# Performance work log

Hardware: AMD Instinct MI355X
Metric: run time of the kernel (lower is better)

Reference implementation:

```python
import jax, jax.numpy as jnp
import numpy as np

NUM_LAYERS = 3
HIDDEN = 64
NUM_CLASSES = 4096
LN_EPS = 1e-5


def setup_inputs() -> dict:
    key = jax.random.key(0)
    ks = jax.random.split(key, 8)
    B, N, E, H = 8, NUM_CLASSES, 131072, HIDDEN
    node_features = jax.random.normal(ks[0], (B, N, H), dtype=jnp.float32)
    edge_indices = jax.random.randint(ks[1], (B, 2, E), 0, N, dtype=jnp.int64)
    edge_attrs = jax.random.normal(ks[2], (B, E, H), dtype=jnp.float32)
    # GraphConvolutionLayer params (xavier_uniform weight, zero bias) per layer
    limit = np.sqrt(6.0 / (H + H)).astype(np.float32)
    W = jax.random.uniform(ks[3], (NUM_LAYERS, H, H), minval=-limit, maxval=limit, dtype=jnp.float32)
    b = jnp.zeros((NUM_LAYERS, H), dtype=jnp.float32)
    gamma = jnp.ones((NUM_LAYERS, H), dtype=jnp.float32)
    beta = jnp.zeros((NUM_LAYERS, H), dtype=jnp.float32)
    global_emb = 0.02 * jax.random.normal(ks[4], (N, H), dtype=jnp.float32)
    return {
        "node_features": node_features,
        "edge_indices": edge_indices,
        "edge_attrs": edge_attrs,
        "W": W,
        "b": b,
        "gamma": gamma,
        "beta": beta,
        "global_emb": global_emb,
    }


def _layer_norm(x, g, bt):
    mu = jnp.mean(x, axis=-1, keepdims=True)
    var = jnp.mean((x - mu) ** 2, axis=-1, keepdims=True)
    return (x - mu) * jax.lax.rsqrt(var + LN_EPS) * g + bt


def reference(node_features, edge_indices, edge_attrs, W, b, gamma, beta, global_emb):
    N = node_features.shape[1]

    def per_graph(x0, ei, ea):
        # presence mask computed on raw node features [N, 1]
        presence = (jnp.sum(x0, axis=1) != 0).astype(x0.dtype)[:, None]
        src, dst = ei[0], ei[1]
        x = x0
        for i in range(NUM_LAYERS):
            residual = x
            h = x @ W[i]                                   # [N, H]
            msg = h[src] * ea                              # gather + edge gate [E, H]
            out = jax.ops.segment_sum(msg, dst, num_segments=N) + b[i]
            out = jax.nn.relu(out)
            out = _layer_norm(out, gamma[i], beta[i])
            x = out + residual if i > 0 else out
        return x * presence + global_emb * (1.0 - presence)

    return jax.vmap(per_graph)(node_features, edge_indices, edge_attrs)
```

## Files before the change

### kernel.cpp

```cpp
#include <hip/hip_runtime.h>

#define GB 8
#define GN 4096
#define GH 64
#define GE 131072
#define LN_EPS 1e-5f
#define NBIN (GB * GN)
#define TOTE (GB * GE)

static __device__ __forceinline__ unsigned short f2bf(float f) {
    union { float f; unsigned int u; } v; v.f = f;
    unsigned int u = v.u;
    return (unsigned short)((u + 0x7FFFu + ((u >> 16) & 1u)) >> 16);
}
static __device__ __forceinline__ void bf2x(unsigned int u, float& lo, float& hi) {
    union { float f; unsigned int i; } a, b;
    a.i = u << 16; b.i = u & 0xFFFF0000u;
    lo = a.f; hi = b.f;
}
static __device__ __forceinline__ void fma8(uint4 ev, uint4 hv, float4& a0, float4& a1) {
    float el, eh, hl, hh;
    bf2x(ev.x, el, eh); bf2x(hv.x, hl, hh);
    a0.x = fmaf(el, hl, a0.x); a0.y = fmaf(eh, hh, a0.y);
    bf2x(ev.y, el, eh); bf2x(hv.y, hl, hh);
    a0.z = fmaf(el, hl, a0.z); a0.w = fmaf(eh, hh, a0.w);
    bf2x(ev.z, el, eh); bf2x(hv.z, hl, hh);
    a1.x = fmaf(el, hl, a1.x); a1.y = fmaf(eh, hh, a1.y);
    bf2x(ev.w, el, eh); bf2x(hv.w, hl, hh);
    a1.z = fmaf(el, hl, a1.z); a1.w = fmaf(eh, hh, a1.w);
}

__global__ void k_init(const float* __restrict__ nf, float* __restrict__ pres) {
    int w = (blockIdx.x * blockDim.x + threadIdx.x) >> 6;
    int lane = threadIdx.x & 63;
    if (w >= NBIN) return;
    float v = nf[(size_t)w * GH + lane];
    #pragma unroll
    for (int o = 1; o < 64; o <<= 1) v += __shfl_xor(v, o, 64);
    if (lane == 0) pres[w] = (v != 0.0f) ? 1.0f : 0.0f;
}

__global__ void k_hist(const int* __restrict__ ei, int* __restrict__ hist) {
    int t = blockIdx.x * blockDim.x + threadIdx.x;
    int b = t >> 17, e = t & (GE - 1);
    int dst = ei[(b << 18) + GE + e];
    atomicAdd(&hist[(b << 12) + dst], 1);
}

__global__ void k_scan(const int* __restrict__ hist, int* __restrict__ off,
                       int* __restrict__ cur) {
    __shared__ int part[256];
    int b = blockIdx.x;
    int t = threadIdx.x;
    int base = (b << 12) + t * 16;
    int c[16];
    int s = 0;
    #pragma unroll
    for (int i = 0; i < 16; ++i) { c[i] = hist[base + i]; s += c[i]; }
    part[t] = s;
    __syncthreads();
    for (int o = 1; o < 256; o <<= 1) {
        int u = (t >= o) ? part[t - o] : 0;
        __syncthreads();
        part[t] += u;
        __syncthreads();
    }
    int p = b * GE + part[t] - s;
    #pragma unroll
    for (int i = 0; i < 16; ++i) { off[base + i] = p; cur[base + i] = p; p += c[i]; }
    if (b == GB - 1 && t == 255) off[NBIN] = TOTE;
}

__global__ void k_fill(const int* __restrict__ ei, int* __restrict__ cur,
                       int* __restrict__ perm, int* __restrict__ sSrc) {
    int t = blockIdx.x * blockDim.x + threadIdx.x;
    int b = t >> 17, e = t & (GE - 1);
    int src = ei[(b << 18) + e];
    int dst = ei[(b << 18) + GE + e];
    int pos = atomicAdd(&cur[(b << 12) + dst], 1);
    perm[pos] = t;
    sSrc[pos] = src;
}

__global__ void k_permcopy(const int* __restrict__ perm, const float* __restrict__ ea,
                           unsigned short* __restrict__ ea_s) {
    int grp = (blockIdx.x * blockDim.x + threadIdx.x) >> 4;
    if (grp >= TOTE) return;
    int sub = threadIdx.x & 15;
    int edge = perm[grp];
    uint4 v = *reinterpret_cast<const uint4*>(ea + ((size_t)edge << 6) + (sub << 2));
    float f0 = __uint_as_float(v.x), f1 = __uint_as_float(v.y);
    float f2 = __uint_as_float(v.z), f3 = __uint_as_float(v.w);
    ushort4 o;
    o.x = f2bf(f0); o.y = f2bf(f1); o.z = f2bf(f2); o.w = f2bf(f3);
    *reinterpret_cast<ushort4*>(ea_s + ((size_t)grp << 6) + (sub << 2)) = o;
}

__global__ void k_gemm(const float* __restrict__ x, const float* __restrict__ W,
                       unsigned short* __restrict__ h, int layer) {
    __shared__ float Wl[GH * GH];
    for (int i = threadIdx.x; i < GH * GH; i += blockDim.x)
        Wl[i] = W[layer * GH * GH + i];
    __syncthreads();
    int w = (blockIdx.x * blockDim.x + threadIdx.x) >> 6;
    int lane = threadIdx.x & 63;
    if (w >= NBIN) return;
    float xv = x[(size_t)w * GH + lane];
    float acc = 0.0f;
    #pragma unroll
    for (int k = 0; k < GH; ++k)
        acc = fmaf(__shfl(xv, k, 64), Wl[k * GH + lane], acc);
    h[(size_t)w * GH + lane] = f2bf(acc);
}

__global__ void k_gather(const int* __restrict__ off, const int* __restrict__ sSrc,
                         const unsigned short* __restrict__ ea_s,
                         const unsigned short* __restrict__ h,
                         const float* __restrict__ bias, const float* __restrict__ gam,
                         const float* __restrict__ bet,
                         float* __restrict__ x, const float* __restrict__ pres,
                         const float* __restrict__ ge, float* __restrict__ out,
                         int layer) {
    int w = (blockIdx.x * blockDim.x + threadIdx.x) >> 6;
    if (w >= NBIN) return;
    int lane = threadIdx.x & 63;
    int g   = lane >> 3;
    int sub = lane & 7;
    int b = w >> 12;
    int beg = off[w], end = off[w + 1];
    const unsigned short* hb = h + ((((size_t)b) << 12) * GH);

    float4 a0 = make_float4(0.f, 0.f, 0.f, 0.f);
    float4 a1 = make_float4(0.f, 0.f, 0.f, 0.f);
    for (int e = beg; e < end; e += 16) {
        int e0 = e + g;
        int e1 = e + 8 + g;
        if (e0 < end) {
            int s0 = sSrc[e0];
            uint4 ev = *reinterpret_cast<const uint4*>(ea_s + (((size_t)e0) << 6) + (sub << 3));
            uint4 hv = *reinterpret_cast<const uint4*>(hb + (((size_t)s0) << 6) + (sub << 3));
            fma8(ev, hv, a0, a1);
        }
        if (e1 < end) {
            int s1 = sSrc[e1];
            uint4 ev = *reinterpret_cast<const uint4*>(ea_s + (((size_t)e1) << 6) + (sub << 3));
            uint4 hv = *reinterpret_cast<const uint4*>(hb + (((size_t)s1) << 6) + (sub << 3));
            fma8(ev, hv, a0, a1);
        }
    }
    #pragma unroll
    for (int o = 8; o < 64; o <<= 1) {
        a0.x += __shfl_xor(a0.x, o, 64);
        a0.y += __shfl_xor(a0.y, o, 64);
        a0.z += __shfl_xor(a0.z, o, 64);
        a0.w += __shfl_xor(a0.w, o, 64);
        a1.x += __shfl_xor(a1.x, o, 64);
        a1.y += __shfl_xor(a1.y, o, 64);
        a1.z += __shfl_xor(a1.z, o, 64);
        a1.w += __shfl_xor(a1.w, o, 64);
    }

    const float4* bias4 = reinterpret_cast<const float4*>(bias + layer * GH + (sub << 3));
    float4 b0 = bias4[0], b1 = bias4[1];
    float4 v0, v1;
    v0.x = fmaxf(a0.x + b0.x, 0.f); v0.y = fmaxf(a0.y + b0.y, 0.f);
    v0.z = fmaxf(a0.z + b0.z, 0.f); v0.w = fmaxf(a0.w + b0.w, 0.f);
    v1.x = fmaxf(a1.x + b1.x, 0.f); v1.y = fmaxf(a1.y + b1.y, 0.f);
    v1.z = fmaxf(a1.z + b1.z, 0.f); v1.w = fmaxf(a1.w + b1.w, 0.f);
    float s = v0.x + v0.y + v0.z + v0.w + v1.x + v1.y + v1.z + v1.w;
    #pragma unroll
    for (int o = 1; o < 8; o <<= 1) s += __shfl_xor(s, o, 64);
    float mu = s * (1.0f / GH);
    float4 d0, d1;
    d0.x = v0.x - mu; d0.y = v0.y - mu; d0.z = v0.z - mu; d0.w = v0.w - mu;
    d1.x = v1.x - mu; d1.y = v1.y - mu; d1.z = v1.z - mu; d1.w = v1.w - mu;
    float q = d0.x*d0.x + d0.y*d0.y + d0.z*d0.z + d0.w*d0.w
            + d1.x*d1.x + d1.y*d1.y + d1.z*d1.z + d1.w*d1.w;
    #pragma unroll
    for (int o = 1; o < 8; o <<= 1) q += __shfl_xor(q, o, 64);
    float r = rsqrtf(q * (1.0f / GH) + LN_EPS);
    const float4* gam4 = reinterpret_cast<const float4*>(gam + layer * GH + (sub << 3));
    const float4* bet4 = reinterpret_cast<const float4*>(bet + layer * GH + (sub << 3));
    float4 g0 = gam4[0], g1 = gam4[1];
    float4 t0 = bet4[0], t1 = bet4[1];
    float4 y0, y1;
    y0.x = d0.x * r * g0.x + t0.x; y0.y = d0.y * r * g0.y + t0.y;
    y0.z = d0.z * r * g0.z + t0.z; y0.w = d0.w * r * g0.w + t0.w;
    y1.x = d1.x * r * g1.x + t1.x; y1.y = d1.y * r * g1.y + t1.y;
    y1.z = d1.z * r * g1.z + t1.z; y1.w = d1.w * r * g1.w + t1.w;

    if (g == 0) {
        float4* xp = reinterpret_cast<float4*>(x + (size_t)w * GH + (sub << 3));
        if (layer > 0) {
            float4 x0 = xp[0], x1 = xp[1];
            y0.x += x0.x; y0.y += x0.y; y0.z += x0.z; y0.w += x0.w;
            y1.x += x1.x; y1.y += x1.y; y1.z += x1.z; y1.w += x1.w;
        }
        if (layer < 2) {
            xp[0] = y0; xp[1] = y1;
        } else {
            float p = pres[w];
            const float4* ge4 = reinterpret_cast<const float4*>(ge + (size_t)(w & (GN - 1)) * GH + (sub << 3));
            float4 e0 = ge4[0], e1 = ge4[1];
            float4 o0, o1;
            o0.x = y0.x * p + e0.x * (1.f - p); o0.y = y0.y * p + e0.y * (1.f - p);
            o0.z = y0.z * p + e0.z * (1.f - p); o0.w = y0.w * p + e0.w * (1.f - p);
            o1.x = y1.x * p + e1.x * (1.f - p); o1.y = y1.y * p + e1.y * (1.f - p);
            o1.z = y1.z * p + e1.z * (1.f - p); o1.w = y1.w * p + e1.w * (1.f - p);
            float4* op = reinterpret_cast<float4*>(out + (size_t)w * GH + (sub << 3));
            op[0] = o0; op[1] = o1;
        }
    }
}

extern "C" void kernel_launch(void* const* d_in, const int* in_sizes, int n_in,
                              void* d_out, int out_size, void* d_ws, size_t ws_size,
                              hipStream_t stream) {
    const float* nf = (const float*)d_in[0];
    const int* ei   = (const int*)d_in[1];
    const float* ea = (const float*)d_in[2];
    const float* W  = (const float*)d_in[3];
    const float* bb = (const float*)d_in[4];
    const float* gg = (const float*)d_in[5];
    const float* be = (const float*)d_in[6];
    const float* ge = (const float*)d_in[7];
    float* out = (float*)d_out;

    float* x    = (float*)d_ws;
    float* pres = x + (size_t)NBIN * GH;
    int* off    = (int*)(pres + NBIN);
    int* cur    = off + NBIN + 1;
    int* hist   = cur + NBIN;
    int* sSrc   = hist + NBIN;
    int* perm   = sSrc + TOTE;
    unsigned short* h_s  = (unsigned short*)(perm + TOTE);
    unsigned short* ea_s = h_s + (size_t)NBIN * GH;

    hipMemsetAsync(hist, 0, NBIN * sizeof(int), stream);
    k_init<<<NBIN / 4, 256, 0, stream>>>(nf, pres);
    k_hist<<<TOTE / 256, 256, 0, stream>>>(ei, hist);
    k_scan<<<GB, 256, 0, stream>>>(hist, off, cur);
    k_fill<<<TOTE / 256, 256, 0, stream>>>(ei, cur, perm, sSrc);
    k_permcopy<<<TOTE / 16, 256, 0, stream>>>(perm, ea, ea_s);

    for (int l = 0; l < 3; ++l) {
        k_gemm<<<NBIN / 4, 256, 0, stream>>>(l == 0 ? nf : x, W, h_s, l);
        k_gather<<<NBIN / 4, 256, 0, stream>>>(off, sSrc, ea_s, h_s, bb, gg, be,
                                               x, pres, ge, out, l);
    }
}
```

Baseline: 427.1 us.

## Replace permuted edge-attr copy with streaming bf16 conversion and indirect gather

Drops the kernel that permuted edge attributes into dst-sorted order. The attributes are instead converted to bf16 in their original order by a coalesced grid-stride kernel. The sort now stores (src, original edge id) pairs, and the gather kernel reads edge attributes indirectly through the original id. This makes the one-time conversion fully coalesced, but the three per-layer gathers now read edge attributes in a scattered rather than sequential pattern.

```diff
diff --git a/kernel.cpp b/kernel.cpp
--- a/kernel.cpp
+++ b/kernel.cpp
@@ -12,6 +12,9 @@
     union { float f; unsigned int u; } v; v.f = f;
     unsigned int u = v.u;
     return (unsigned short)((u + 0x7FFFu + ((u >> 16) & 1u)) >> 16);
+}
+static __device__ __forceinline__ unsigned int f2bf2(float lo, float hi) {
+    return (unsigned int)f2bf(lo) | ((unsigned int)f2bf(hi) << 16);
 }
 static __device__ __forceinline__ void bf2x(unsigned int u, float& lo, float& hi) {
     union { float f; unsigned int i; } a, b;
@@ -72,28 +75,28 @@
 }
 
 __global__ void k_fill(const int* __restrict__ ei, int* __restrict__ cur,
-                       int* __restrict__ perm, int* __restrict__ sSrc) {
+                       int2* __restrict__ sPair) {
     int t = blockIdx.x * blockDim.x + threadIdx.x;
     int b = t >> 17, e = t & (GE - 1);
     int src = ei[(b << 18) + e];
     int dst = ei[(b << 18) + GE + e];
     int pos = atomicAdd(&cur[(b << 12) + dst], 1);
-    perm[pos] = t;
-    sSrc[pos] = src;
-}
-
-__global__ void k_permcopy(const int* __restrict__ perm, const float* __restrict__ ea,
-                           unsigned short* __restrict__ ea_s) {
-    int grp = (blockIdx.x * blockDim.x + threadIdx.x) >> 4;
-    if (grp >= TOTE) return;
-    int sub = threadIdx.x & 15;
-    int edge = perm[grp];
-    uint4 v = *reinterpret_cast<const uint4*>(ea + ((size_t)edge << 6) + (sub << 2));
-    float f0 = __uint_as_float(v.x), f1 = __uint_as_float(v.y);
-    float f2 = __uint_as_float(v.z), f3 = __uint_as_float(v.w);
-    ushort4 o;
-    o.x = f2bf(f0); o.y = f2bf(f1); o.z = f2bf(f2); o.w = f2bf(f3);
-    *reinterpret_cast<ushort4*>(ea_s + ((size_t)grp << 6) + (sub << 2)) = o;
+    sPair[pos] = make_int2(src, t);
+}
+
+__global__ void k_conv(const float4* __restrict__ ea4, uint4* __restrict__ ea_b) {
+    const int n = TOTE * GH / 8;
+    int stride = gridDim.x * blockDim.x;
+    for (int i = blockIdx.x * blockDim.x + threadIdx.x; i < n; i += stride) {
+        float4 lo = ea4[2 * i];
+        float4 hi = ea4[2 * i + 1];
+        uint4 o;
+        o.x = f2bf2(lo.x, lo.y);
+        o.y = f2bf2(lo.z, lo.w);
+        o.z = f2bf2(hi.x, hi.y);
+        o.w = f2bf2(hi.z, hi.w);
+        ea_b[i] = o;
+    }
 }
 
 __global__ void k_gemm(const float* __restrict__ x, const float* __restrict__ W,
@@ -113,8 +116,8 @@
     h[(size_t)w * GH + lane] = f2bf(acc);
 }
 
-__global__ void k_gather(const int* __restrict__ off, const int* __restrict__ sSrc,
-                         const unsigned short* __restrict__ ea_s,
+__global__ void k_gather(const int* __restrict__ off, const int2* __restrict__ sPair,
+                         const unsigned short* __restrict__ ea_b,
                          const unsigned short* __restrict__ h,
                          const float* __restrict__ bias, const float* __restrict__ gam,
                          const float* __restrict__ bet,
@@ -136,15 +139,15 @@
         int e0 = e + g;
         int e1 = e + 8 + g;
         if (e0 < end) {
-            int s0 = sSrc[e0];
-            uint4 ev = *reinterpret_cast<const uint4*>(ea_s + (((size_t)e0) << 6) + (sub << 3));
-            uint4 hv = *reinterpret_cast<const uint4*>(hb + (((size_t)s0) << 6) + (sub << 3));
+            int2 p0 = sPair[e0];
+            uint4 ev = *reinterpret_cast<const uint4*>(ea_b + (((size_t)p0.y) << 6) + (sub << 3));
+            uint4 hv = *reinterpret_cast<const uint4*>(hb + (((size_t)p0.x) << 6) + (sub << 3));
             fma8(ev, hv, a0, a1);
         }
         if (e1 < end) {
-            int s1 = sSrc[e1];
-            uint4 ev = *reinterpret_cast<const uint4*>(ea_s + (((size_t)e1) << 6) + (sub << 3));
-            uint4 hv = *reinterpret_cast<const uint4*>(hb + (((size_t)s1) << 6) + (sub << 3));
+            int2 p1 = sPair[e1];
+            uint4 ev = *reinterpret_cast<const uint4*>(ea_b + (((size_t)p1.y) << 6) + (sub << 3));
+            uint4 hv = *reinterpret_cast<const uint4*>(hb + (((size_t)p1.x) << 6) + (sub << 3));
             fma8(ev, hv, a0, a1);
         }
     }
@@ -231,21 +234,20 @@
     int* off    = (int*)(pres + NBIN);
     int* cur    = off + NBIN + 1;
     int* hist   = cur + NBIN;
-    int* sSrc   = hist + NBIN;
-    int* perm   = sSrc + TOTE;
-    unsigned short* h_s  = (unsigned short*)(perm + TOTE);
-    unsigned short* ea_s = h_s + (size_t)NBIN * GH;
+    int2* sPair = (int2*)(hist + NBIN);
+    unsigned short* h_s  = (unsigned short*)(sPair + TOTE);
+    unsigned short* ea_b = h_s + (size_t)NBIN * GH;
 
     hipMemsetAsync(hist, 0, NBIN * sizeof(int), stream);
     k_init<<<NBIN / 4, 256, 0, stream>>>(nf, pres);
     k_hist<<<TOTE / 256, 256, 0, stream>>>(ei, hist);
     k_scan<<<GB, 256, 0, stream>>>(hist, off, cur);
-    k_fill<<<TOTE / 256, 256, 0, stream>>>(ei, cur, perm, sSrc);
-    k_permcopy<<<TOTE / 16, 256, 0, stream>>>(perm, ea, ea_s);
+    k_fill<<<TOTE / 256, 256, 0, stream>>>(ei, cur, sPair);
+    k_conv<<<2048, 256, 0, stream>>>((const float4*)ea, (uint4*)ea_b);
 
     for (int l = 0; l < 3; ++l) {
         k_gemm<<<NBIN / 4, 256, 0, stream>>>(l == 0 ? nf : x, W, h_s, l);
-        k_gather<<<NBIN / 4, 256, 0, stream>>>(off, sSrc, ea_s, h_s, bb, gg, be,
+        k_gather<<<NBIN / 4, 256, 0, stream>>>(off, sPair, ea_b, h_s, bb, gg, be,
                                                x, pres, ge, out, l);
     }
 }
```

After: 465.0 us. 8.9% more time.
